# Performance work log

Measured on AMD Instinct MI355X. Metric: run time of the kernel, lower is better.

The kernel has to match this reference:

```python
import jax, jax.numpy as jnp
import numpy as np

# module hyperparameters (init_kwargs); topk=-1 is unused by forward
DILATION, SUBSIZE, ANGLE = 4, 16, 4
FLT_MAX = float(np.finfo(np.float32).max)


def _rot_grid(h, w, angle_deg):
    # cv2.warpAffine with M = cv2.getRotationMatrix2D((w/2, h/2), angle, 1)
    # samples the SOURCE at the inverse rotation (rotate dst coords by +angle
    # about the center used by the module, which is (w/2, h/2), not (w-1)/2).
    cx, cy = w / 2.0, h / 2.0
    t = np.deg2rad(angle_deg)
    ca, sa = np.cos(t), np.sin(t)
    xs, ys = np.meshgrid(np.arange(w, dtype=np.float32), np.arange(h, dtype=np.float32))
    sx = ca * xs - sa * ys + (1.0 - ca) * cx + sa * cy
    sy = sa * xs + ca * ys - sa * cx + (1.0 - ca) * cy
    return jnp.asarray(sx, jnp.float32), jnp.asarray(sy, jnp.float32)


def _bilinear(img, sx, sy):
    # img [..., H, W]; bilinear sample with zero border (cv2 BORDER_CONSTANT)
    H, W = img.shape[-2], img.shape[-1]
    x0f, y0f = jnp.floor(sx), jnp.floor(sy)
    wx1, wy1 = sx - x0f, sy - y0f
    wx0, wy0 = 1.0 - wx1, 1.0 - wy1
    x0, y0 = x0f.astype(jnp.int32), y0f.astype(jnp.int32)

    def gather(xi, yi):
        valid = ((xi >= 0) & (xi < W) & (yi >= 0) & (yi < H)).astype(img.dtype)
        v = img[..., jnp.clip(yi, 0, H - 1), jnp.clip(xi, 0, W - 1)]
        return v * valid

    return (wy0 * wx0 * gather(x0, y0) + wy0 * wx1 * gather(x0 + 1, y0)
            + wy1 * wx0 * gather(x0, y0 + 1) + wy1 * wx1 * gather(x0 + 1, y0 + 1))


def _forward(fm1, fm2):
    bs, c, h, w = fm1.shape  # module assumes c == 1 (squeezes channel dim)
    d = min(h, w, DILATION)
    ss = min(h, w, SUBSIZE)
    fm2 = jax.lax.stop_gradient(fm2)  # torch detaches ref2 before warpAffine
    grids = [_rot_grid(ss, ss, a) for a in range(-ANGLE, ANGLE + 1)]
    # rotated validity mask (warped all-ones image), same for every block
    masks = [_bilinear(jnp.ones((ss, ss), fm1.dtype), gx, gy) for gx, gy in grids]
    total = jnp.zeros((bs,), fm1.dtype)
    for sub_x in range(0, w, ss):
        for sub_y in range(0, h, ss):
            r1 = fm1[:, 0, sub_y:sub_y + ss, sub_x:sub_x + ss]  # [bs,ss,ss]
            # the nested border-case slicing is exactly a clamp of the start index
            starts = [(int(np.clip(sub_y + dh, 0, h - ss)), int(np.clip(sub_x + dw, 0, w - ss)))
                      for dw in range(-d, d + 1) for dh in range(-d, d + 1)]
            blocks = jnp.stack([fm2[:, 0, y0:y0 + ss, x0:x0 + ss] for (y0, x0) in starts])  # [S,bs,ss,ss]
            sub_min = jnp.full((bs,), FLT_MAX, fm1.dtype)
            for (gx, gy), m in zip(grids, masks):
                r_blocks = _bilinear(blocks, gx, gy)        # [S,bs,ss,ss] rotated candidates
                se = (r1[None] - r_blocks) ** 2 * m          # masked squared error
                rands = se.sum((-1, -2)) / m.sum()           # [S,bs] rotate_mse_loss
                sub_min = jnp.minimum(sub_min, rands.min(0))
            total = total + sub_min
    return total


def setup_inputs():
    key = jax.random.key(0)
    k1, k2 = jax.random.split(key)
    fm1 = jax.random.normal(k1, (1024, 1, 64, 64), jnp.float32)
    fm2 = jax.random.normal(k2, (1024, 1, 64, 64), jnp.float32)
    return {"fm1": fm1, "fm2": fm2}


def reference(fm1, fm2):
    return _forward(fm1, fm2)
```

## Files before the change

### kernel.cpp

```cpp
#include <hip/hip_runtime.h>
#include <hip/hip_fp16.h>
#include <math.h>

#define NANG 9
#define SS 16
#define NPIX 256
#define WSH 72
#define NROWW 70
#define WINSZH (NROWW * WSH)
#define NITEM (NANG * 16)
#define IPW (NITEM / 4)
#define FLTMAX_BITS 0x7F7FFFFFu


__global__ __launch_bounds__(256) void build_table(uint4* __restrict__ tbl)
{
    __shared__ float red[256];
    const int p  = threadIdx.x;
    const int px = p & 15, py = p >> 4;
    for (int a = 0; a < NANG; ++a) {
        double t  = (double)(a - 4) * 0.017453292519943295;
        double ca = cos(t), sa = sin(t);
        float sx = (float)(ca * px - sa * py + (1.0 - ca) * 8.0 + sa * 8.0);
        float sy = (float)(sa * px + ca * py - sa * 8.0 + (1.0 - ca) * 8.0);
        float x0f = floorf(sx), y0f = floorf(sy);
        int   x0  = (int)x0f,   y0  = (int)y0f;
        float wx1 = sx - x0f, wx0 = 1.0f - wx1;
        float wy1 = sy - y0f, wy0 = 1.0f - wy1;
        float ewx0 = (x0 >= 0 && x0 < SS)         ? wx0 : 0.0f;
        float ewx1 = (x0 + 1 >= 0 && x0 + 1 < SS) ? wx1 : 0.0f;
        float ewy0 = (y0 >= 0 && y0 < SS)         ? wy0 : 0.0f;
        float ewy1 = (y0 + 1 >= 0 && y0 + 1 < SS) ? wy1 : 0.0f;
        float m = (ewx0 + ewx1) * (ewy0 + ewy1);

        red[p] = m;
        __syncthreads();
        for (int s = 128; s > 0; s >>= 1) {
            if (p < s) red[p] += red[p + s];
            __syncthreads();
        }
        float msum = red[0];
        __syncthreads();

        float sc = sqrtf(m / msum);
        x0 = max(-1, min(15, x0));
        y0 = max(-1, min(15, y0));
        uint4 e;
        e.x = (unsigned)__half_as_ushort(__float2half(ewx0)) |
              ((unsigned)__half_as_ushort(__float2half(ewx1)) << 16);
        e.y = (unsigned)__half_as_ushort(__float2half(-sc * ewy0)) |
              ((unsigned)__half_as_ushort(__float2half(-sc * ewy1)) << 16);
        e.z = __float_as_uint(sc);
        e.w = (unsigned)((y0 + 1) * WSH + (x0 + 1));
        tbl[a * NPIX + p] = e;
    }
}

#define DPPADD(v, ctrl, rmask)                                                   \
    v += __int_as_float(__builtin_amdgcn_update_dpp(                             \
            0, __float_as_int(v), ctrl, rmask, 0xf, true))

template<int NP>
__device__ __forceinline__ void rowload(const __half2* __restrict__ winh,
                                        int (&addr)[4],
                                        const __half2 (&wx0)[4], const __half2 (&wx1)[4],
                                        __half2 (&h)[4][NP])
{
    #pragma unroll
    for (int k = 0; k < 4; ++k) {
        __half2 d[2 * NP];
        #pragma unroll
        for (int j = 0; j < 2 * NP; ++j) d[j] = winh[addr[k] + j];
        #pragma unroll
        for (int c = 0; c < NP; ++c)
            h[k][c] = __hfma2(wx1[k], d[2 * c + 1], __hmul2(wx0[k], d[2 * c]));
        addr[k] += WSH;
    }
}

template<int NP>
__device__ __forceinline__ void bystep(const __half2 (&hp)[4][NP], const __half2 (&hc)[4][NP],
                                       const __half2 (&wy0n)[4], const __half2 (&wy1n)[4],
                                       const __half2 (&r1s)[4],
                                       unsigned* __restrict__ sm, int lane)
{
    __half2 acc[NP];
    #pragma unroll
    for (int c = 0; c < NP; ++c) acc[c] = __floats2half2_rn(0.f, 0.f);
    #pragma unroll
    for (int k = 0; k < 4; ++k) {
        #pragma unroll
        for (int c = 0; c < NP; ++c) {
            __half2 e = __hfma2(wy0n[k], hp[k][c], r1s[k]);
            e = __hfma2(wy1n[k], hc[k][c], e);
            acc[c] = __hfma2(e, e, acc[c]);
        }
    }
    constexpr int NJ = 2 * NP - 1;
    float v[NJ];
    #pragma unroll
    for (int c = 0; c < NP; ++c) {
        v[2 * c] = __low2float(acc[c]);
        if (2 * c + 1 < NJ) v[2 * c + 1] = __high2float(acc[c]);
    }
    #pragma unroll
    for (int j = 0; j < NJ; ++j) {
        DPPADD(v[j], 0xB1,  0xf);
        DPPADD(v[j], 0x4E,  0xf);
        DPPADD(v[j], 0x141, 0xf);
        DPPADD(v[j], 0x140, 0xf);
        DPPADD(v[j], 0x142, 0xa);
        DPPADD(v[j], 0x143, 0xc);
    }
    if (lane == 63) {
        float best = v[0];
        #pragma unroll
        for (int j = 1; j < NJ; ++j) best = fminf(best, v[j]);
        atomicMin(sm, __float_as_uint(best));
    }
}

template<int NBY, int NP>
__device__ __forceinline__ void proc(const __half2* __restrict__ winh, int (&addr)[4],
                                     const __half2 (&wx0)[4], const __half2 (&wx1)[4],
                                     const __half2 (&wy0n)[4], const __half2 (&wy1n)[4],
                                     const __half2 (&r1s)[4],
                                     unsigned* __restrict__ sm, int lane)
{
    __half2 hA[4][NP], hB[4][NP];
    rowload<NP>(winh, addr, wx0, wx1, hA);
    #pragma unroll
    for (int by = 0; by < NBY + 1; by += 2) {
        rowload<NP>(winh, addr, wx0, wx1, hB);
        bystep<NP>(hA, hB, wy0n, wy1n, r1s, sm, lane);
        if (by + 1 < NBY + 1) {
            rowload<NP>(winh, addr, wx0, wx1, hA);
            bystep<NP>(hB, hA, wy0n, wy1n, r1s, sm, lane);
        }
    }
}

__global__ __launch_bounds__(256) void randip_main(const float* __restrict__ fm1,
                                                   const float* __restrict__ fm2,
                                                   const uint4* __restrict__ gt,
                                                   float* __restrict__ out)
{
    __shared__ __half2 winh[WINSZH];
    __shared__ unsigned submin[16];

    const int b    = blockIdx.x;
    const int tid  = threadIdx.x;
    const int wave = tid >> 6;
    const int lane = tid & 63;

    for (int i = tid; i < WINSZH; i += 256) winh[i] = __floats2half2_rn(0.f, 0.f);
    if (tid < 16) submin[tid] = FLTMAX_BITS;
    __syncthreads();

    const float* img2 = fm2 + (size_t)b * 4096;
    for (int i = tid; i < 64 * 65; i += 256) {
        int r = i / 65, c = i - r * 65;
        float lo = (c >= 1)  ? img2[r * 64 + c - 1] : 0.f;
        float hi = (c <= 63) ? img2[r * 64 + c]     : 0.f;
        winh[(r + 1) * WSH + c] = __floats2half2_rn(lo, hi);
    }
    __syncthreads();

    const float* img1 = fm1 + (size_t)b * 4096;

    int a_cur = -1;
    __half2 wx0[4], wx1[4], wy0n[4], wy1n[4], r1s[4];
    float   sca[4];
    int     off[4];

    for (int i = wave * IPW; i < (wave + 1) * IPW; ++i) {
        const int a = i >> 4, sub = i & 15;
        if (a != a_cur) {
            a_cur = a;
            const uint4* tp = gt + a * NPIX + lane;
            #pragma unroll
            for (int k = 0; k < 4; ++k) {
                uint4 te = tp[64 * k];
                __half2 X = *(const __half2*)&te.x;
                __half2 Y = *(const __half2*)&te.y;
                wx0[k]  = __half2half2(__low2half(X));
                wx1[k]  = __half2half2(__high2half(X));
                wy0n[k] = __half2half2(__low2half(Y));
                wy1n[k] = __half2half2(__high2half(Y));
                sca[k]  = __uint_as_float(te.z);
                off[k]  = (int)te.w;
            }
        }
        const int sub_x = (sub & 3) << 4;
        const int sub_y = (sub >> 2) << 4;
        const int x_lo = max(sub_x - 4, 0);
        const int y_lo = max(sub_y - 4, 0);
        const int nvx = min(sub_x + 4, 48) - x_lo;
        const int nby = min(sub_y + 4, 48) - y_lo;
        const int rowbase0 = y_lo * WSH + x_lo;

        const float* r1p = img1 + (sub_y + (lane >> 4)) * 64 + sub_x + (lane & 15);
        #pragma unroll
        for (int k = 0; k < 4; ++k)
            r1s[k] = __float2half2_rn(sca[k] * r1p[k * 4 * 64]);

        int addr[4];
        #pragma unroll
        for (int k = 0; k < 4; ++k) addr[k] = rowbase0 + off[k];

        unsigned* sm = &submin[sub];
        if (nby == 8) {
            if (nvx == 8) proc<8, 5>(winh, addr, wx0, wx1, wy0n, wy1n, r1s, sm, lane);
            else          proc<8, 3>(winh, addr, wx0, wx1, wy0n, wy1n, r1s, sm, lane);
        } else {
            if (nvx == 8) proc<4, 5>(winh, addr, wx0, wx1, wy0n, wy1n, r1s, sm, lane);
            else          proc<4, 3>(winh, addr, wx0, wx1, wy0n, wy1n, r1s, sm, lane);
        }
    }
    __syncthreads();

    if (tid == 0) {
        float t = 0.0f;
        #pragma unroll
        for (int s = 0; s < 16; ++s) t += __uint_as_float(submin[s]);
        out[b] = t;
    }
}

extern "C" void kernel_launch(void* const* d_in, const int* in_sizes, int n_in,
                              void* d_out, int out_size, void* d_ws, size_t ws_size,
                              hipStream_t stream)
{
    const float* fm1 = (const float*)d_in[0];
    const float* fm2 = (const float*)d_in[1];
    float* out = (float*)d_out;
    uint4* tbl = (uint4*)d_ws;

    const int nb = in_sizes[0] >> 12;

    hipLaunchKernelGGL(build_table, dim3(1), dim3(256), 0, stream, tbl);
    hipLaunchKernelGGL(randip_main, dim3(nb), dim3(256), 0, stream, fm1, fm2, tbl, out);
}
```

Baseline: 367.5 us.

## Split each image across four blocks by sub-row band with partial-sum reduction

Each image is now handled by four blocks, one per 16-row band of sub-blocks. Each block stages only the 27 needed rows of fm2 into a smaller shared window instead of the whole image. Four times as many smaller-LDS blocks with occupancy hint 8 should raise occupancy and parallelism, and a small reduce kernel then sums the four partials. The cost is one extra launch, some redundant loads of the overlapping halo rows, and a workspace partial buffer.

```diff
diff --git a/kernel.cpp b/kernel.cpp
--- a/kernel.cpp
+++ b/kernel.cpp
@@ -6,11 +6,10 @@
 #define SS 16
 #define NPIX 256
 #define WSH 72
-#define NROWW 70
-#define WINSZH (NROWW * WSH)
-#define NITEM (NANG * 16)
-#define IPW (NITEM / 4)
+#define WROWS 27
+#define WINSZH (WROWS * WSH)
 #define FLTMAX_BITS 0x7F7FFFFFu
+#define PART_BYTES 16384
 
 
 __global__ __launch_bounds__(256) void build_table(uint4* __restrict__ tbl)
@@ -140,29 +139,39 @@
     }
 }
 
-__global__ __launch_bounds__(256) void randip_main(const float* __restrict__ fm1,
-                                                   const float* __restrict__ fm2,
-                                                   const uint4* __restrict__ gt,
-                                                   float* __restrict__ out)
+__global__ __launch_bounds__(256, 8) void randip_main(const float* __restrict__ fm1,
+                                                      const float* __restrict__ fm2,
+                                                      const uint4* __restrict__ gt,
+                                                      float* __restrict__ part)
 {
     __shared__ __half2 winh[WINSZH];
-    __shared__ unsigned submin[16];
-
-    const int b    = blockIdx.x;
+    __shared__ unsigned submin[4];
+
+    const int bi   = blockIdx.x;
+    const int b    = bi >> 2;
+    const int g    = bi & 3;
     const int tid  = threadIdx.x;
     const int wave = tid >> 6;
     const int lane = tid & 63;
 
+    const int sub_y  = g << 4;
+    const int y_lo   = max(sub_y - 4, 0);
+    const int nby    = min(sub_y + 4, 48) - y_lo;
+    const int base_y = y_lo - 1;
+
     for (int i = tid; i < WINSZH; i += 256) winh[i] = __floats2half2_rn(0.f, 0.f);
-    if (tid < 16) submin[tid] = FLTMAX_BITS;
+    if (tid < 4) submin[tid] = FLTMAX_BITS;
     __syncthreads();
 
     const float* img2 = fm2 + (size_t)b * 4096;
-    for (int i = tid; i < 64 * 65; i += 256) {
+    for (int i = tid; i < WROWS * 65; i += 256) {
         int r = i / 65, c = i - r * 65;
-        float lo = (c >= 1)  ? img2[r * 64 + c - 1] : 0.f;
-        float hi = (c <= 63) ? img2[r * 64 + c]     : 0.f;
-        winh[(r + 1) * WSH + c] = __floats2half2_rn(lo, hi);
+        int gr = base_y + r;
+        if (gr >= 0 && gr <= 63) {
+            float lo = (c >= 1)  ? img2[gr * 64 + c - 1] : 0.f;
+            float hi = (c <= 63) ? img2[gr * 64 + c]     : 0.f;
+            winh[r * WSH + c] = __floats2half2_rn(lo, hi);
+        }
     }
     __syncthreads();
 
@@ -173,8 +182,8 @@
     float   sca[4];
     int     off[4];
 
-    for (int i = wave * IPW; i < (wave + 1) * IPW; ++i) {
-        const int a = i >> 4, sub = i & 15;
+    for (int i = wave * 9; i < wave * 9 + 9; ++i) {
+        const int a = i >> 2, sc = i & 3;
         if (a != a_cur) {
             a_cur = a;
             const uint4* tp = gt + a * NPIX + lane;
@@ -191,13 +200,9 @@
                 off[k]  = (int)te.w;
             }
         }
-        const int sub_x = (sub & 3) << 4;
-        const int sub_y = (sub >> 2) << 4;
+        const int sub_x = sc << 4;
         const int x_lo = max(sub_x - 4, 0);
-        const int y_lo = max(sub_y - 4, 0);
         const int nvx = min(sub_x + 4, 48) - x_lo;
-        const int nby = min(sub_y + 4, 48) - y_lo;
-        const int rowbase0 = y_lo * WSH + x_lo;
 
         const float* r1p = img1 + (sub_y + (lane >> 4)) * 64 + sub_x + (lane & 15);
         #pragma unroll
@@ -206,9 +211,9 @@
 
         int addr[4];
         #pragma unroll
-        for (int k = 0; k < 4; ++k) addr[k] = rowbase0 + off[k];
-
-        unsigned* sm = &submin[sub];
+        for (int k = 0; k < 4; ++k) addr[k] = off[k] + x_lo;
+
+        unsigned* sm = &submin[sc];
         if (nby == 8) {
             if (nvx == 8) proc<8, 5>(winh, addr, wx0, wx1, wy0n, wy1n, r1s, sm, lane);
             else          proc<8, 3>(winh, addr, wx0, wx1, wy0n, wy1n, r1s, sm, lane);
@@ -222,9 +227,17 @@
     if (tid == 0) {
         float t = 0.0f;
         #pragma unroll
-        for (int s = 0; s < 16; ++s) t += __uint_as_float(submin[s]);
-        out[b] = t;
-    }
+        for (int s = 0; s < 4; ++s) t += __uint_as_float(submin[s]);
+        part[b * 4 + g] = t;
+    }
+}
+
+__global__ __launch_bounds__(256) void reduce_out(const float* __restrict__ part,
+                                                  float* __restrict__ out, int nb)
+{
+    int i = blockIdx.x * 256 + threadIdx.x;
+    if (i < nb)
+        out[i] = ((part[4 * i] + part[4 * i + 1]) + part[4 * i + 2]) + part[4 * i + 3];
 }
 
 extern "C" void kernel_launch(void* const* d_in, const int* in_sizes, int n_in,
@@ -233,11 +246,15 @@
 {
     const float* fm1 = (const float*)d_in[0];
     const float* fm2 = (const float*)d_in[1];
-    float* out = (float*)d_out;
-    uint4* tbl = (uint4*)d_ws;
+    float* out  = (float*)d_out;
+    float* part = (float*)d_ws;
+    uint4* tbl  = (uint4*)((char*)d_ws + PART_BYTES);
 
     const int nb = in_sizes[0] >> 12;
 
     hipLaunchKernelGGL(build_table, dim3(1), dim3(256), 0, stream, tbl);
-    hipLaunchKernelGGL(randip_main, dim3(nb), dim3(256), 0, stream, fm1, fm2, tbl, out);
-}
+    hipLaunchKernelGGL(randip_main, dim3(4 * nb), dim3(256), 0, stream,
+                       fm1, fm2, tbl, part);
+    hipLaunchKernelGGL(reduce_out, dim3((nb + 255) / 256), dim3(256), 0, stream,
+                       part, out, nb);
+}
```

New measurement: 504.9 us. 37.4% more time.
